# Optimization experiments

Hardware: AMD Instinct MI355X
Metric: run time of the kernel (lower is better)

The kernel has to match this reference:

```python
import jax, jax.numpy as jnp
import numpy as np

# --- static problem geometry (compile-time constants, as in MinkowskiEngine decompositions) ---
N_TOTAL = 500000          # total points across all clouds
C = 128                   # feature channels
G = 32                    # GroupNorm groups
EPS = 1e-5                # torch GroupNorm default
LENGTHS = np.array([40000, 55000, 70000, 45000, 80000, 65000, 90000, 55000])  # points per cloud
assert LENGTHS.sum() == N_TOTAL
B = len(LENGTHS)
SEG = np.repeat(np.arange(B), LENGTHS)  # [N] cloud id for each position of the concatenated permutation


def setup_inputs() -> dict:
    key = jax.random.key(0)
    k1, k2, k3, k4 = jax.random.split(key, 4)
    feats = jax.random.normal(k1, (N_TOTAL, C), dtype=jnp.float32)   # x.F
    # concatenated decomposition_permutations: a permutation of arange(N)
    perm = jax.random.permutation(k2, N_TOTAL).astype(jnp.int64)
    gamma = 1.0 + 0.1 * jax.random.normal(k3, (C,), dtype=jnp.float32)  # GroupNorm weight
    beta = 0.1 * jax.random.normal(k4, (C,), dtype=jnp.float32)         # GroupNorm bias
    return {"feats": feats, "gamma": gamma, "beta": beta, "perm": perm}


def reference(feats, gamma, beta, perm):
    Cg = C // G
    seg = jnp.asarray(SEG)                              # [N]
    x = feats[perm]                                     # [N, C] per-cloud gather (concatenated)
    xg = x.reshape(-1, G, Cg)                           # [N, G, Cg]
    # per-(cloud, group) statistics over all points of the cloud and channels of the group
    s = jax.ops.segment_sum(xg.sum(-1), seg, num_segments=B)            # [B, G]
    ss = jax.ops.segment_sum((xg * xg).sum(-1), seg, num_segments=B)    # [B, G]
    cnt = jnp.asarray(LENGTHS * Cg, dtype=feats.dtype)[:, None]          # [B, 1]
    mean = s / cnt
    var = ss / cnt - mean * mean
    inv = jax.lax.rsqrt(var + EPS)                      # [B, G]
    xn = (xg - mean[seg][:, :, None]) * inv[seg][:, :, None]             # [N, G, Cg]
    y = xn.reshape(-1, C) * gamma + beta                # [N, C] affine per channel
    # scatter back via inverse permutation: out[perm[i]] = y[i]
    out = jnp.zeros_like(y).at[perm].set(y)
    return out
```

## Files before the change

kernel.cpp:

```cpp
#include <hip/hip_runtime.h>

#define N_TOTAL 500000
#define C 128
#define G 32
#define NB 8
#define EPS 1e-5f
#define NBLK 2048

typedef float f4 __attribute__((ext_vector_type(4)));

__device__ __forceinline__ int cloud_of(int i) {
    int c = 0;
    c += (i >= 40000);
    c += (i >= 95000);
    c += (i >= 165000);
    c += (i >= 210000);
    c += (i >= 290000);
    c += (i >= 355000);
    c += (i >= 445000);
    return c;
}

__device__ const float d_cnt[NB] = {160000.f, 220000.f, 280000.f, 180000.f,
                                    320000.f, 260000.f, 360000.f, 220000.f};


__global__ __launch_bounds__(256) void gn_prep(const int* __restrict__ perm,
                                               unsigned char* __restrict__ cid,
                                               float* __restrict__ ws) {
    int gid = blockIdx.x * 256 + threadIdx.x;
    if (gid < 2 * NB * G) ws[gid] = 0.f;
    int stride = gridDim.x * 256;
    for (int i = gid; i < N_TOTAL; i += stride)
        cid[perm[i]] = (unsigned char)cloud_of(i);
}

__global__ __launch_bounds__(256) void gn_stats(const float* __restrict__ feats,
                                                const unsigned char* __restrict__ cid,
                                                float* __restrict__ ws,
                                                int rows_per_block) {
    __shared__ float lacc[2 * NB * G];
    int tid = threadIdx.x;
    for (int k = tid; k < 2 * NB * G; k += 256) lacc[k] = 0.f;
    __syncthreads();

    const int g = tid & 31;
    const int rsub = tid >> 5;
    int start = blockIdx.x * rows_per_block;
    int end = start + rows_per_block;
    if (end > N_TOTAL) end = N_TOTAL;

    float s[NB], ss[NB];
#pragma unroll
    for (int b = 0; b < NB; b++) { s[b] = 0.f; ss[b] = 0.f; }

    for (int row = start + rsub; row < end; row += 8) {
        int cl = cid[row];
        f4 v = ((const f4*)(feats + ((long long)row << 7)))[g];
        float rs = v.x + v.y + v.z + v.w;
        float rss = v.x * v.x + v.y * v.y + v.z * v.z + v.w * v.w;
#pragma unroll
        for (int b = 0; b < NB; b++) {
            if (cl == b) { s[b] += rs; ss[b] += rss; }
        }
    }
#pragma unroll
    for (int b = 0; b < NB; b++) {
        if (s[b] != 0.f || ss[b] != 0.f) {
            atomicAdd(&lacc[b * G + g], s[b]);
            atomicAdd(&lacc[NB * G + b * G + g], ss[b]);
        }
    }
    __syncthreads();

    for (int k = tid; k < 2 * NB * G; k += 256) {
        float a = lacc[k];
        if (a != 0.f) atomicAdd(&ws[k], a);
    }
}

__global__ __launch_bounds__(256) void gn_apply(const float* __restrict__ feats,
                                                const unsigned char* __restrict__ cid,
                                                const float* __restrict__ gamma,
                                                const float* __restrict__ beta,
                                                const float* __restrict__ ws,
                                                float* __restrict__ out,
                                                int rows_per_block) {
    __shared__ float lmean[NB * G];
    __shared__ float linv[NB * G];
    int tid = threadIdx.x;
    {
        float sm = ws[tid];
        float sq = ws[NB * G + tid];
        float cnt = d_cnt[tid >> 5];
        float m = sm / cnt;
        float var = sq / cnt - m * m;
        lmean[tid] = m;
        linv[tid] = rsqrtf(var + EPS);
    }
    __syncthreads();

    const int g = tid & 31;
    const int rsub = tid >> 5;
    f4 gm = ((const f4*)gamma)[g];
    f4 bt = ((const f4*)beta)[g];

    int start = blockIdx.x * rows_per_block;
    int end = start + rows_per_block;
    if (end > N_TOTAL) end = N_TOTAL;

    for (int row = start + rsub; row < end; row += 8) {
        int cl = cid[row];
        f4 v = ((const f4*)(feats + ((long long)row << 7)))[g];
        float m = lmean[cl * G + g];
        float inv = linv[cl * G + g];
        f4 y;
        y.x = (v.x - m) * inv * gm.x + bt.x;
        y.y = (v.y - m) * inv * gm.y + bt.y;
        y.z = (v.z - m) * inv * gm.z + bt.z;
        y.w = (v.w - m) * inv * gm.w + bt.w;
        __builtin_nontemporal_store(y, (f4*)(out + ((long long)row << 7)) + g);
    }
}

extern "C" void kernel_launch(void* const* d_in, const int* in_sizes, int n_in,
                              void* d_out, int out_size, void* d_ws, size_t ws_size,
                              hipStream_t stream) {
    const float* feats = (const float*)d_in[0];
    const float* gamma = (const float*)d_in[1];
    const float* beta  = (const float*)d_in[2];
    const int*   perm  = (const int*)d_in[3];
    float* out = (float*)d_out;
    float* ws  = (float*)d_ws;
    unsigned char* cid = (unsigned char*)d_ws + 4096;

    gn_prep<<<512, 256, 0, stream>>>(perm, cid, ws);

    int rpb = (N_TOTAL + NBLK - 1) / NBLK;
    gn_stats<<<NBLK, 256, 0, stream>>>(feats, cid, ws, rpb);
    gn_apply<<<NBLK, 256, 0, stream>>>(feats, cid, gamma, beta, ws, out, rpb);
}
```

Baseline: 171.2 us.

## Fuse prep, stats and apply into one cooperative kernel with grid syncs

Merges the three kernels (cloud-id scatter, per-group statistics, normalize/apply) into a single cooperative launch that uses grid-wide barriers between phases, with 1024 persistent blocks of 256 threads each. This removes two kernel launches and their gaps, and lets each block reread its own row range of feats in the apply phase while it may still be in cache. In exchange it adds grid.sync overhead, caps the grid at the co-resident block count, and a cooperative launch can fail if occupancy is insufficient.

```diff
diff --git a/kernel.cpp b/kernel.cpp
--- a/kernel.cpp
+++ b/kernel.cpp
@@ -1,11 +1,15 @@
 #include <hip/hip_runtime.h>
+#include <hip/hip_cooperative_groups.h>
+
+namespace cg = cooperative_groups;
 
 #define N_TOTAL 500000
 #define C 128
 #define G 32
 #define NB 8
 #define EPS 1e-5f
-#define NBLK 2048
+#define NBLOCKS 1024
+#define RPB ((N_TOTAL + NBLOCKS - 1) / NBLOCKS)
 
 typedef float f4 __attribute__((ext_vector_type(4)));
 
@@ -24,30 +28,31 @@
 __device__ const float d_cnt[NB] = {160000.f, 220000.f, 280000.f, 180000.f,
                                     320000.f, 260000.f, 360000.f, 220000.f};
 
+__global__ __launch_bounds__(256, 4) void gn_fused(const float* __restrict__ feats,
+                                                   const float* __restrict__ gamma,
+                                                   const float* __restrict__ beta,
+                                                   const int* __restrict__ perm,
+                                                   float* __restrict__ ws,
+                                                   unsigned char* __restrict__ cid,
+                                                   float* __restrict__ out) {
+    cg::grid_group grid = cg::this_grid();
+    const int tid = threadIdx.x;
+    const int gid = blockIdx.x * 256 + tid;
 
-__global__ __launch_bounds__(256) void gn_prep(const int* __restrict__ perm,
-                                               unsigned char* __restrict__ cid,
-                                               float* __restrict__ ws) {
-    int gid = blockIdx.x * 256 + threadIdx.x;
     if (gid < 2 * NB * G) ws[gid] = 0.f;
-    int stride = gridDim.x * 256;
-    for (int i = gid; i < N_TOTAL; i += stride)
+    for (int i = gid; i < N_TOTAL; i += NBLOCKS * 256)
         cid[perm[i]] = (unsigned char)cloud_of(i);
-}
 
-__global__ __launch_bounds__(256) void gn_stats(const float* __restrict__ feats,
-                                                const unsigned char* __restrict__ cid,
-                                                float* __restrict__ ws,
-                                                int rows_per_block) {
+    grid.sync();
+
     __shared__ float lacc[2 * NB * G];
-    int tid = threadIdx.x;
     for (int k = tid; k < 2 * NB * G; k += 256) lacc[k] = 0.f;
     __syncthreads();
 
     const int g = tid & 31;
     const int rsub = tid >> 5;
-    int start = blockIdx.x * rows_per_block;
-    int end = start + rows_per_block;
+    int start = blockIdx.x * RPB;
+    int end = start + RPB;
     if (end > N_TOTAL) end = N_TOTAL;
 
     float s[NB], ss[NB];
@@ -77,18 +82,11 @@
         float a = lacc[k];
         if (a != 0.f) atomicAdd(&ws[k], a);
     }
-}
 
-__global__ __launch_bounds__(256) void gn_apply(const float* __restrict__ feats,
-                                                const unsigned char* __restrict__ cid,
-                                                const float* __restrict__ gamma,
-                                                const float* __restrict__ beta,
-                                                const float* __restrict__ ws,
-                                                float* __restrict__ out,
-                                                int rows_per_block) {
+    grid.sync();
+
     __shared__ float lmean[NB * G];
     __shared__ float linv[NB * G];
-    int tid = threadIdx.x;
     {
         float sm = ws[tid];
         float sq = ws[NB * G + tid];
@@ -100,14 +98,8 @@
     }
     __syncthreads();
 
-    const int g = tid & 31;
-    const int rsub = tid >> 5;
     f4 gm = ((const f4*)gamma)[g];
     f4 bt = ((const f4*)beta)[g];
-
-    int start = blockIdx.x * rows_per_block;
-    int end = start + rows_per_block;
-    if (end > N_TOTAL) end = N_TOTAL;
 
     for (int row = start + rsub; row < end; row += 8) {
         int cl = cid[row];
@@ -134,9 +126,8 @@
     float* ws  = (float*)d_ws;
     unsigned char* cid = (unsigned char*)d_ws + 4096;
 
-    gn_prep<<<512, 256, 0, stream>>>(perm, cid, ws);
-
-    int rpb = (N_TOTAL + NBLK - 1) / NBLK;
-    gn_stats<<<NBLK, 256, 0, stream>>>(feats, cid, ws, rpb);
-    gn_apply<<<NBLK, 256, 0, stream>>>(feats, cid, gamma, beta, ws, out, rpb);
+    void* args[] = {(void*)&feats, (void*)&gamma, (void*)&beta, (void*)&perm,
+                    (void*)&ws, (void*)&cid, (void*)&out};
+    hipLaunchCooperativeKernel((const void*)gn_fused, dim3(NBLOCKS), dim3(256),
+                               args, 0, stream);
 }
```

Result: slower. 324.9 us (+89.8%).
